# Kernel optimization log

Measured on AMD Instinct MI355X. Metric: run time of the kernel, lower is better.

Reference implementation:

```python
import jax, jax.numpy as jnp
import numpy as np

LN_EPS = 1e-6

def _layernorm(x, g, b):
    mu = jnp.mean(x, axis=-1, keepdims=True)
    var = jnp.mean((x - mu) ** 2, axis=-1, keepdims=True)
    return (x - mu) / jnp.sqrt(var + LN_EPS) * g + b

def _mha(q, k, v, wq, bq, wk, bk, wv, bv, fc, fcb, ln_g, ln_b, n_head, d_k, d_v):
    # standard post-LN multi-head attention (residual + layernorm), eval mode (no dropout)
    b, lq, _ = q.shape
    bk_, lk, _ = k.shape
    residual = q
    qh = (q @ wq + bq).reshape(b, lq, n_head, d_k).transpose(0, 2, 1, 3)      # [b,h,lq,dk]
    kh = (k @ wk + bk).reshape(bk_, lk, n_head, d_k).transpose(0, 2, 1, 3)    # [bk,h,lk,dk]
    vh = (v @ wv + bv).reshape(bk_, lk, n_head, d_v).transpose(0, 2, 1, 3)    # [bk,h,lk,dv]
    attn = jax.nn.softmax(jnp.matmul(qh, kh.swapaxes(-1, -2)) / (d_k ** 0.5), axis=-1)  # [b,h,lq,lk]
    out = jnp.matmul(attn, vh)                                                # [b,h,lq,dv]
    out = out.transpose(0, 2, 1, 3).reshape(b, lq, n_head * d_v)
    pre = out
    out = _layernorm(out @ fc + fcb + residual, ln_g, ln_b)
    return out, attn, pre


def setup_inputs() -> dict:
    key = jax.random.key(0)
    ks = jax.random.split(key, 32)
    B, C, H, W = 16, 64, 32, 32
    NC, D = 5, 96  # num_classes, memory feature dim
    s = 0.05
    d = {
        'x': jax.random.normal(ks[0], (B, C, H, W), jnp.float32),
        'memory': jax.random.normal(ks[1], (NC, D), jnp.float32),
        'wb_w': jax.random.normal(ks[2], (C, NC), jnp.float32) * s,
        'wb_b': jnp.zeros((NC,), jnp.float32),
        # slf_attn: n_head=1, d_model=64, d_input_k=96, d_k=96, d_v=64
        'a1_wq': jax.random.normal(ks[3], (64, 96), jnp.float32) * s,
        'a1_bq': jnp.zeros((96,), jnp.float32),
        'a1_wk': jax.random.normal(ks[4], (96, 96), jnp.float32) * s,
        'a1_bk': jnp.zeros((96,), jnp.float32),
        'a1_wv': jax.random.normal(ks[5], (96, 64), jnp.float32) * s,
        'a1_bv': jnp.zeros((64,), jnp.float32),
        'a1_fc': jax.random.normal(ks[6], (64, 64), jnp.float32) * s,
        'a1_fcb': jnp.zeros((64,), jnp.float32),
        'a1_ln_g': jnp.ones((64,), jnp.float32),
        'a1_ln_b': jnp.zeros((64,), jnp.float32),
        # slf_attn1: n_head=4, d_model=64, d_input_k=64, d_k=64, d_v=64
        'a2_wq': jax.random.normal(ks[7], (64, 256), jnp.float32) * s,
        'a2_bq': jnp.zeros((256,), jnp.float32),
        'a2_wk': jax.random.normal(ks[8], (64, 256), jnp.float32) * s,
        'a2_bk': jnp.zeros((256,), jnp.float32),
        'a2_wv': jax.random.normal(ks[9], (64, 256), jnp.float32) * s,
        'a2_bv': jnp.zeros((256,), jnp.float32),
        'a2_fc': jax.random.normal(ks[10], (256, 64), jnp.float32) * s,
        'a2_fcb': jnp.zeros((64,), jnp.float32),
        'a2_ln_g': jnp.ones((64,), jnp.float32),
        'a2_ln_b': jnp.zeros((64,), jnp.float32),
    }
    return d


def reference(x, memory, wb_w, wb_b,
              a1_wq, a1_bq, a1_wk, a1_bk, a1_wv, a1_bv, a1_fc, a1_fcb, a1_ln_g, a1_ln_b,
              a2_wq, a2_bq, a2_wk, a2_bk, a2_wv, a2_bv, a2_fc, a2_fcb, a2_ln_g, a2_ln_b):
    b, c, H, W = x.shape
    xt = x.transpose(0, 2, 3, 1).reshape(b, H * W, c)            # [b,HW,64]
    weight = xt @ wb_w + wb_b                                    # [b,HW,5]
    weight1 = jax.nn.softmax(weight, axis=-1)                    # softmax over classes
    weight2 = jax.nn.softmax(weight.transpose(0, 2, 1), axis=-1) # [b,5,HW], softmax over HW
    class_feat1 = jnp.matmul(weight2, xt)                        # [b,5,64] class-weighted pooling
    mem = memory[None]                                           # [1,5,96]
    cf, _, _ = _mha(class_feat1, mem, mem,
                    a1_wq, a1_bq, a1_wk, a1_bk, a1_wv, a1_bv, a1_fc, a1_fcb, a1_ln_g, a1_ln_b,
                    n_head=1, d_k=96, d_v=64)                    # [b,5,64]
    cf = jnp.matmul(weight1, cf)                                 # redistribution [b,HW,64]
    cf, _, _ = _mha(cf, cf, cf,
                    a2_wq, a2_bq, a2_wk, a2_bk, a2_wv, a2_bv, a2_fc, a2_fcb, a2_ln_g, a2_ln_b,
                    n_head=4, d_k=64, d_v=64)                    # [b,HW,64]
    return cf.transpose(0, 2, 1).reshape(-1, 64, H, W)           # [b,64,H,W]
```

## Files before the change

kernel.cpp:

```cpp
#include <hip/hip_runtime.h>
#include <math.h>

typedef unsigned short ushort_t;
typedef __attribute__((ext_vector_type(8))) short short8;
typedef __attribute__((ext_vector_type(4))) float f32x4;

#define B_  16
#define HW_ 1024
#define C_  64
#define NC_ 5
#define D1_ 96
#define NH_ 4
#define DH_ 64

#define MFMA32(A,B,C) __builtin_amdgcn_mfma_f32_16x16x32_bf16(A,B,C,0,0,0)

__device__ __forceinline__ ushort_t f2bf(float f) {
    unsigned u = __float_as_uint(f);
    u = u + 0x7fffu + ((u >> 16) & 1u);
    return (ushort_t)(u >> 16);
}

__device__ __forceinline__ unsigned pack2_trunc(float lo, float hi) {
    return (__float_as_uint(hi) & 0xffff0000u) | (__float_as_uint(lo) >> 16);
}
__device__ __forceinline__ float bf_lo(unsigned u) { return __uint_as_float(u << 16); }
__device__ __forceinline__ float bf_hi(unsigned u) { return __uint_as_float(u & 0xffff0000u); }

__global__ __launch_bounds__(64) void k1_logits(const float* __restrict__ x,
                                                const float* __restrict__ wb_w,
                                                const float* __restrict__ wb_b,
                                                float* __restrict__ logitsT,
                                                float* __restrict__ w1) {
    int b = blockIdx.x >> 4;
    int hw = (blockIdx.x & 15) * 64 + threadIdx.x;
    const float* xb = x + (size_t)b * C_ * HW_;
    float acc[NC_];
#pragma unroll
    for (int j = 0; j < NC_; j++) acc[j] = wb_b[j];
#pragma unroll 8
    for (int c = 0; c < C_; c++) {
        float xv = xb[c * HW_ + hw];
#pragma unroll
        for (int j = 0; j < NC_; j++) acc[j] += xv * wb_w[c * NC_ + j];
    }
    float m = acc[0];
#pragma unroll
    for (int j = 1; j < NC_; j++) m = fmaxf(m, acc[j]);
    float e[NC_], s = 0.f;
#pragma unroll
    for (int j = 0; j < NC_; j++) { e[j] = __expf(acc[j] - m); s += e[j]; }
    float inv = 1.f / s;
    int idx = b * HW_ + hw;
#pragma unroll
    for (int j = 0; j < NC_; j++) {
        logitsT[((size_t)b * NC_ + j) * HW_ + hw] = acc[j];
        w1[(size_t)idx * NC_ + j] = e[j] * inv;
    }
}

__global__ __launch_bounds__(256) void k2b_pool(const float* __restrict__ x,
                                                const float* __restrict__ logitsT,
                                                float* __restrict__ cf1) {
    __shared__ float pl[NC_ * HW_];
    __shared__ float sinv[NC_];
    int t = threadIdx.x;
    int b = blockIdx.x >> 4, chg = blockIdx.x & 15;
    const float* lp = logitsT + (size_t)b * NC_ * HW_;
    for (int i = t * 4; i < NC_ * HW_; i += 1024)
        *(float4*)(pl + i) = *(const float4*)(lp + i);
    __syncthreads();
    int w = t >> 6, lane = t & 63;
    for (int r = w; r < NC_; r += 4) {
        float m = -1e30f;
        for (int i = lane; i < HW_; i += 64) m = fmaxf(m, pl[r * HW_ + i]);
#pragma unroll
        for (int off = 1; off < 64; off <<= 1) m = fmaxf(m, __shfl_xor(m, off, 64));
        float s = 0.f;
        for (int i = lane; i < HW_; i += 64) {
            float e = __expf(pl[r * HW_ + i] - m);
            pl[r * HW_ + i] = e;
            s += e;
        }
#pragma unroll
        for (int off = 1; off < 64; off <<= 1) s += __shfl_xor(s, off, 64);
        if (lane == 0) sinv[r] = 1.f / s;
    }
    __syncthreads();
    int ch = chg * 4 + w;
    const float* xc = x + ((size_t)b * C_ + ch) * HW_;
    float acc[NC_] = {0.f, 0.f, 0.f, 0.f, 0.f};
#pragma unroll
    for (int i = 0; i < HW_ / 64; i++) {
        int hw = i * 64 + lane;
        float xv = xc[hw];
#pragma unroll
        for (int c = 0; c < NC_; c++) acc[c] += xv * pl[c * HW_ + hw];
    }
#pragma unroll
    for (int c = 0; c < NC_; c++) {
        float a = acc[c];
#pragma unroll
        for (int off = 1; off < 64; off <<= 1) a += __shfl_xor(a, off, 64);
        if (lane == 0) cf1[((size_t)b * NC_ + c) * C_ + ch] = a * sinv[c];
    }
}

__global__ __launch_bounds__(256) void k3_mha1(const float* __restrict__ cf1,
                                               const float* __restrict__ wq, const float* __restrict__ bq,
                                               const float* __restrict__ mem,
                                               const float* __restrict__ wk, const float* __restrict__ bk,
                                               const float* __restrict__ wv, const float* __restrict__ bv,
                                               const float* __restrict__ fc, const float* __restrict__ fcb,
                                               const float* __restrict__ lng, const float* __restrict__ lnb,
                                               float* __restrict__ cfs) {
    __shared__ float cs[NC_ * C_];
    __shared__ float kh[NC_ * D1_];
    __shared__ float vh[NC_ * DH_];
    __shared__ float q[NC_ * D1_];
    __shared__ float sc[NC_ * NC_];
    __shared__ float pp[NC_ * NC_];
    __shared__ float o[NC_ * C_];
    __shared__ float z[NC_ * C_];
    __shared__ float mu[NC_], rs[NC_];
    int t = threadIdx.x, b = blockIdx.x;
    for (int i = t; i < NC_ * C_; i += 256) cs[i] = cf1[(size_t)b * NC_ * C_ + i];
    for (int idx = t; idx < NC_ * D1_; idx += 256) {
        int i = idx / D1_, k = idx % D1_;
        float a = bk[k];
        for (int d = 0; d < D1_; d++) a += mem[i * D1_ + d] * wk[d * D1_ + k];
        kh[idx] = a;
    }
    for (int idx = t; idx < NC_ * DH_; idx += 256) {
        int i = idx / DH_, dv = idx % DH_;
        float a = bv[dv];
        for (int d = 0; d < D1_; d++) a += mem[i * D1_ + d] * wv[d * DH_ + dv];
        vh[idx] = a;
    }
    __syncthreads();
    for (int idx = t; idx < NC_ * D1_; idx += 256) {
        int i = idx / D1_, k = idx % D1_;
        float a = bq[k];
        for (int c = 0; c < C_; c++) a += cs[i * C_ + c] * wq[c * D1_ + k];
        q[idx] = a;
    }
    __syncthreads();
    if (t < NC_ * NC_) {
        int i = t / NC_, j = t % NC_;
        float a = 0.f;
        for (int k = 0; k < D1_; k++) a += q[i * D1_ + k] * kh[j * D1_ + k];
        sc[t] = a * 0.1020620726159657f;
    }
    __syncthreads();
    if (t < NC_) {
        float m = sc[t * NC_];
        for (int j = 1; j < NC_; j++) m = fmaxf(m, sc[t * NC_ + j]);
        float e[NC_], s = 0.f;
        for (int j = 0; j < NC_; j++) { e[j] = __expf(sc[t * NC_ + j] - m); s += e[j]; }
        float inv = 1.f / s;
        for (int j = 0; j < NC_; j++) pp[t * NC_ + j] = e[j] * inv;
    }
    __syncthreads();
    for (int idx = t; idx < NC_ * C_; idx += 256) {
        int i = idx / C_, dv = idx % C_;
        float a = 0.f;
        for (int j = 0; j < NC_; j++) a += pp[i * NC_ + j] * vh[j * C_ + dv];
        o[idx] = a;
    }
    __syncthreads();
    for (int idx = t; idx < NC_ * C_; idx += 256) {
        int i = idx / C_, dd = idx % C_;
        float a = fcb[dd] + cs[idx];
        for (int c2 = 0; c2 < C_; c2++) a += o[i * C_ + c2] * fc[c2 * C_ + dd];
        z[idx] = a;
    }
    __syncthreads();
    if (t < NC_) {
        float s = 0.f;
        for (int d = 0; d < C_; d++) s += z[t * C_ + d];
        float mm = s / C_;
        float v = 0.f;
        for (int d = 0; d < C_; d++) { float dd2 = z[t * C_ + d] - mm; v += dd2 * dd2; }
        mu[t] = mm; rs[t] = rsqrtf(v / C_ + 1e-6f);
    }
    __syncthreads();
    for (int idx = t; idx < NC_ * C_; idx += 256) {
        int i = idx / C_, dd = idx % C_;
        cfs[(size_t)b * NC_ * C_ + idx] = (z[idx] - mu[i]) * rs[i] * lng[dd] + lnb[dd];
    }
}

__global__ __launch_bounds__(256) void k5_proj(const float* __restrict__ w1,
                                               const float* __restrict__ cfs,
                                               const float* __restrict__ wq, const float* __restrict__ bq,
                                               const float* __restrict__ wk, const float* __restrict__ bk,
                                               const float* __restrict__ wv, const float* __restrict__ bv,
                                               ushort_t* __restrict__ Qb, ushort_t* __restrict__ Kb,
                                               ushort_t* __restrict__ Vt) {
    __shared__ float rows[8][64];
    int t = threadIdx.x;
    int which = blockIdx.y;
    int m0 = blockIdx.x * 8;
    int b5 = m0 >> 10;
    {
        int ch = t & 63, rr = t >> 6;
        const float* cp = cfs + (size_t)b5 * NC_ * C_;
        for (int r = rr; r < 8; r += 4) {
            const float* w1p = w1 + (size_t)(m0 + r) * NC_;
            float a = 0.f;
#pragma unroll
            for (int c = 0; c < NC_; c++) a += w1p[c] * cp[c * 64 + ch];
            rows[r][ch] = a;
        }
    }
    __syncthreads();
    const float* W = (which == 0) ? wq : (which == 1) ? wk : wv;
    const float* bias = (which == 0) ? bq : (which == 1) ? bk : bv;
    float scale = (which == 0) ? 0.18033688011112042f : 1.0f;
    int c = t;
    float bb = bias[c];
    float acc[8];
#pragma unroll
    for (int r = 0; r < 8; r++) acc[r] = bb;
    for (int k = 0; k < 64; k++) {
        float wv_ = W[k * 256 + c];
#pragma unroll
        for (int r = 0; r < 8; r++) acc[r] += rows[r][k] * wv_;
    }
    int h = c >> 6, dd = c & 63;
    if (which == 2) {
        union { ushort_t s[8]; uint4 u; } pk;
#pragma unroll
        for (int r = 0; r < 8; r++) pk.s[r] = f2bf(acc[r]);
        int l0 = m0 & 1023;
        *(uint4*)(Vt + ((size_t)(b5 * NH_ + h) * DH_ + dd) * HW_ + l0) = pk.u;
    } else {
        ushort_t* dst = (which == 0) ? Qb : Kb;
#pragma unroll
        for (int r = 0; r < 8; r++) {
            int m = m0 + r, b = m >> 10, hw = m & 1023;
            dst[(((size_t)(b * NH_ + h) * HW_) + hw) * DH_ + dd] = f2bf(acc[r] * scale);
        }
    }
}

__global__ __launch_bounds__(256) void k6_attn(const ushort_t* __restrict__ Qb,
                                               const ushort_t* __restrict__ Kb,
                                               const ushort_t* __restrict__ Vt,
                                               ushort_t* __restrict__ aoP0, ushort_t* __restrict__ aoP1,
                                               float* __restrict__ sP0, float* __restrict__ sP1) {
    int t = threadIdx.x;
    int w = t >> 6;
    int lane = t & 63;
    int l15 = lane & 15;
    int quad = lane >> 4;
    int L = blockIdx.x;
    int bh = ((L >> 3) & 7) * 8 + (L & 7);
    int khalf = (L >> 6) & 1;
    int qt = L >> 7;
    int b = bh >> 2, h = bh & 3;
    const ushort_t* Qp = Qb + (size_t)bh * HW_ * DH_;
    const ushort_t* Kp = Kb + (size_t)bh * HW_ * DH_;
    const ushort_t* Vp = Vt + (size_t)bh * DH_ * HW_;
    int row0 = qt * 256 + w * 16;
    short8 q0[4], q1[4];
#pragma unroll
    for (int tl = 0; tl < 4; tl++) {
        const ushort_t* qp = Qp + (size_t)(row0 + tl * 64 + l15) * DH_ + quad * 8;
        q0[tl] = *(const short8*)(qp);
        q1[tl] = *(const short8*)(qp + 32);
    }
    int f0 = ((l15 >> 2) * 8) + (l15 & 3);
    int kstart = khalf * 512;
    const ushort_t* K0p = Kp + (size_t)(kstart + f0) * DH_ + quad * 8;
    const ushort_t* K1p = Kp + (size_t)(kstart + f0 + 4) * DH_ + quad * 8;
    const ushort_t* Vp0 = Vp + (size_t)(0 * 16 + l15) * HW_ + kstart + quad * 8;
    const ushort_t* Vp1 = Vp + (size_t)(1 * 16 + l15) * HW_ + kstart + quad * 8;
    const ushort_t* Vp2 = Vp + (size_t)(2 * 16 + l15) * HW_ + kstart + quad * 8;
    const ushort_t* Vp3 = Vp + (size_t)(3 * 16 + l15) * HW_ + kstart + quad * 8;
    const short ONE = (short)0x3F80;
    short8 ones = {ONE, ONE, ONE, ONE, ONE, ONE, ONE, ONE};
    f32x4 o0[4], o1[4], o2[4], o3[4], oS[4];
#pragma unroll
    for (int tl = 0; tl < 4; tl++) {
        o0[tl] = (f32x4){0,0,0,0}; o1[tl] = (f32x4){0,0,0,0};
        o2[tl] = (f32x4){0,0,0,0}; o3[tl] = (f32x4){0,0,0,0};
        oS[tl] = (f32x4){0,0,0,0};
    }
    for (int kt = 0; kt < 16; kt++) {
        int kbase = kt * 32;
        size_t koff = (size_t)kbase * DH_;
        short8 ka0 = *(const short8*)(K0p + koff);
        short8 ka1 = *(const short8*)(K0p + koff + 32);
        short8 kb0 = *(const short8*)(K1p + koff);
        short8 kb1 = *(const short8*)(K1p + koff + 32);
        short8 v0 = *(const short8*)(Vp0 + kbase);
        short8 v1 = *(const short8*)(Vp1 + kbase);
        short8 v2 = *(const short8*)(Vp2 + kbase);
        short8 v3 = *(const short8*)(Vp3 + kbase);
        f32x4 z = {0,0,0,0};
#pragma unroll
        for (int tl = 0; tl < 4; tl++) {
            f32x4 s0 = MFMA32(ka0, q0[tl], z);  s0 = MFMA32(ka1, q1[tl], s0);
            f32x4 s1 = MFMA32(kb0, q0[tl], z);  s1 = MFMA32(kb1, q1[tl], s1);
            float p0 = exp2f(s0[0]), p1 = exp2f(s0[1]), p2 = exp2f(s0[2]), p3 = exp2f(s0[3]);
            float p4 = exp2f(s1[0]), p5 = exp2f(s1[1]), p6 = exp2f(s1[2]), p7 = exp2f(s1[3]);
            union { short8 v; unsigned u[4]; } pf;
            pf.u[0] = pack2_trunc(p0, p1);  pf.u[1] = pack2_trunc(p2, p3);
            pf.u[2] = pack2_trunc(p4, p5);  pf.u[3] = pack2_trunc(p6, p7);
            o0[tl] = MFMA32(v0, pf.v, o0[tl]);
            o1[tl] = MFMA32(v1, pf.v, o1[tl]);
            o2[tl] = MFMA32(v2, pf.v, o2[tl]);
            o3[tl] = MFMA32(v3, pf.v, o3[tl]);
            oS[tl] = MFMA32(ones, pf.v, oS[tl]);
        }
    }
    ushort_t* aoP = khalf ? aoP1 : aoP0;
    float* sP = khalf ? sP1 : sP0;
#pragma unroll
    for (int tl = 0; tl < 4; tl++) {
        int rowg = row0 + tl * 64 + l15;
        ushort_t* aop = aoP + ((size_t)(b * HW_ + rowg)) * 256 + h * 64 + quad * 4;
        uint2 u;
        u.x = pack2_trunc(o0[tl][0], o0[tl][1]); u.y = pack2_trunc(o0[tl][2], o0[tl][3]);
        *(uint2*)(aop + 0) = u;
        u.x = pack2_trunc(o1[tl][0], o1[tl][1]); u.y = pack2_trunc(o1[tl][2], o1[tl][3]);
        *(uint2*)(aop + 16) = u;
        u.x = pack2_trunc(o2[tl][0], o2[tl][1]); u.y = pack2_trunc(o2[tl][2], o2[tl][3]);
        *(uint2*)(aop + 32) = u;
        u.x = pack2_trunc(o3[tl][0], o3[tl][1]); u.y = pack2_trunc(o3[tl][2], o3[tl][3]);
        *(uint2*)(aop + 48) = u;
        if (quad == 0)
            sP[(size_t)(b * HW_ + rowg) * NH_ + h] = oS[tl][0];
    }
}

__global__ __launch_bounds__(256) void k7_final(const ushort_t* __restrict__ aoP0,
                                                const ushort_t* __restrict__ aoP1,
                                                const float* __restrict__ sP0,
                                                const float* __restrict__ sP1,
                                                const float* __restrict__ w1,
                                                const float* __restrict__ cfs,
                                                const float* __restrict__ fc, const float* __restrict__ fcb,
                                                const float* __restrict__ lng, const float* __restrict__ lnb,
                                                float* __restrict__ out) {
    __shared__ float srow[16 * 256];
    __shared__ float rinv[64];
    __shared__ float T[64 * 17];
    int t = threadIdx.x, w = t >> 6, d = t & 63;
    int m0 = blockIdx.x * 16;
    int b = m0 >> 10;
    if (t < 64) {
        int row = t >> 2, hh = t & 3;
        float s = sP0[(size_t)(m0 + row) * NH_ + hh] + sP1[(size_t)(m0 + row) * NH_ + hh];
        rinv[t] = 1.f / s;
    }
    __syncthreads();
    for (int i = t; i < 512; i += 256) {
        uint4 a  = *(const uint4*)(aoP0 + (size_t)m0 * 256 + i * 8);
        uint4 c4 = *(const uint4*)(aoP1 + (size_t)m0 * 256 + i * 8);
        int e = i * 8, row = e >> 8, hh = (e >> 6) & 3;
        float r = rinv[row * 4 + hh];
        srow[e + 0] = (bf_lo(a.x) + bf_lo(c4.x)) * r;
        srow[e + 1] = (bf_hi(a.x) + bf_hi(c4.x)) * r;
        srow[e + 2] = (bf_lo(a.y) + bf_lo(c4.y)) * r;
        srow[e + 3] = (bf_hi(a.y) + bf_hi(c4.y)) * r;
        srow[e + 4] = (bf_lo(a.z) + bf_lo(c4.z)) * r;
        srow[e + 5] = (bf_hi(a.z) + bf_hi(c4.z)) * r;
        srow[e + 6] = (bf_lo(a.w) + bf_lo(c4.w)) * r;
        srow[e + 7] = (bf_hi(a.w) + bf_hi(c4.w)) * r;
    }
    __syncthreads();
    float bias = fcb[d];
    const float* cp = cfs + (size_t)b * NC_ * C_;
    float a[4];
#pragma unroll
    for (int j = 0; j < 4; j++) {
        int m = m0 + w * 4 + j;
        const float* w1p = w1 + (size_t)m * NC_;
        float acc = bias;
#pragma unroll
        for (int c = 0; c < NC_; c++) acc += w1p[c] * cp[c * 64 + d];
        a[j] = acc;
    }
#pragma unroll 8
    for (int k = 0; k < 256; k++) {
        float f = fc[k * 64 + d];
#pragma unroll
        for (int j = 0; j < 4; j++) a[j] += srow[(w * 4 + j) * 256 + k] * f;
    }
    float g = lng[d], be = lnb[d];
#pragma unroll
    for (int j = 0; j < 4; j++) {
        float s1 = a[j], s2 = a[j] * a[j];
#pragma unroll
        for (int off = 1; off < 64; off <<= 1) {
            s1 += __shfl_xor(s1, off, 64);
            s2 += __shfl_xor(s2, off, 64);
        }
        float mu = s1 * (1.f / 64.f);
        float var = s2 * (1.f / 64.f) - mu * mu;
        float rstd = rsqrtf(var + 1e-6f);
        T[d * 17 + w * 4 + j] = (a[j] - mu) * rstd * g + be;
    }
    __syncthreads();
    int ch = t >> 2, part = t & 3;
    int hw0 = m0 & 1023;
    float4 v = {T[ch * 17 + part * 4 + 0], T[ch * 17 + part * 4 + 1],
                T[ch * 17 + part * 4 + 2], T[ch * 17 + part * 4 + 3]};
    *(float4*)&out[((size_t)b * 64 + ch) * 1024 + hw0 + part * 4] = v;
}

extern "C" void kernel_launch(void* const* d_in, const int* in_sizes, int n_in,
                              void* d_out, int out_size, void* d_ws, size_t ws_size,
                              hipStream_t stream) {
    const float* x      = (const float*)d_in[0];
    const float* memory = (const float*)d_in[1];
    const float* wb_w   = (const float*)d_in[2];
    const float* wb_b   = (const float*)d_in[3];
    const float* a1_wq  = (const float*)d_in[4];
    const float* a1_bq  = (const float*)d_in[5];
    const float* a1_wk  = (const float*)d_in[6];
    const float* a1_bk  = (const float*)d_in[7];
    const float* a1_wv  = (const float*)d_in[8];
    const float* a1_bv  = (const float*)d_in[9];
    const float* a1_fc  = (const float*)d_in[10];
    const float* a1_fcb = (const float*)d_in[11];
    const float* a1_ln_g = (const float*)d_in[12];
    const float* a1_ln_b = (const float*)d_in[13];
    const float* a2_wq  = (const float*)d_in[14];
    const float* a2_bq  = (const float*)d_in[15];
    const float* a2_wk  = (const float*)d_in[16];
    const float* a2_bk  = (const float*)d_in[17];
    const float* a2_wv  = (const float*)d_in[18];
    const float* a2_bv  = (const float*)d_in[19];
    const float* a2_fc  = (const float*)d_in[20];
    const float* a2_fcb = (const float*)d_in[21];
    const float* a2_ln_g = (const float*)d_in[22];
    const float* a2_ln_b = (const float*)d_in[23];

    float* ws = (float*)d_ws;
    float* logitsT = ws;
    float* w1  = logitsT + 81920;
    float* cf1 = w1 + 81920;
    float* cfs = cf1 + 5120;
    float* sP0 = cfs + 5120;
    float* sP1 = sP0 + 65536;
    ushort_t* aoP0 = (ushort_t*)(sP1 + 65536);
    ushort_t* aoP1 = aoP0 + 4194304;
    ushort_t* Qb = aoP1 + 4194304;
    ushort_t* Kb = Qb + 4194304;
    ushort_t* Vt = Kb + 4194304;

    k1_logits<<<256, 64, 0, stream>>>(x, wb_w, wb_b, logitsT, w1);
    k2b_pool<<<256, 256, 0, stream>>>(x, logitsT, cf1);
    k3_mha1<<<16, 256, 0, stream>>>(cf1, a1_wq, a1_bq, memory, a1_wk, a1_bk,
                                    a1_wv, a1_bv, a1_fc, a1_fcb,
                                    a1_ln_g, a1_ln_b, cfs);
    k5_proj<<<dim3(2048, 3), 256, 0, stream>>>(w1, cfs, a2_wq, a2_bq, a2_wk, a2_bk,
                                               a2_wv, a2_bv, Qb, Kb, Vt);
    k6_attn<<<512, 256, 0, stream>>>(Qb, Kb, Vt, aoP0, aoP1, sP0, sP1);
    k7_final<<<1024, 256, 0, stream>>>(aoP0, aoP1, sP0, sP1, w1, cfs, a2_fc, a2_fcb,
                                       a2_ln_g, a2_ln_b, (float*)d_out);
}
```

Before: 223.8 us.

## Rewrite QKV projection with bf16 MFMA tiles and vectorize fc reduction

Replaces the scalar FP32 QKV projection kernel, which handled 8 rows per block, with an MFMA-based kernel that handles 64 rows per block. Each block stages the redistributed activations and a bf16-transposed weight tile in shared memory, then issues 16x16x32 bf16 MFMAs, using a transposed operand arrangement for V so it can write Vt directly. Separately, the final kernel's fc reduction now reads srow as float4 and four fc values per step. The projection inputs are now rounded to bf16 before the matmul, which loses some precision, and each block reloads and converts the full weight matrix.

```diff
diff --git a/kernel.cpp b/kernel.cpp
--- a/kernel.cpp
+++ b/kernel.cpp
@@ -23,6 +23,9 @@
 
 __device__ __forceinline__ unsigned pack2_trunc(float lo, float hi) {
     return (__float_as_uint(hi) & 0xffff0000u) | (__float_as_uint(lo) >> 16);
+}
+__device__ __forceinline__ unsigned pack2_rne(float lo, float hi) {
+    return ((unsigned)f2bf(hi) << 16) | (unsigned)f2bf(lo);
 }
 __device__ __forceinline__ float bf_lo(unsigned u) { return __uint_as_float(u << 16); }
 __device__ __forceinline__ float bf_hi(unsigned u) { return __uint_as_float(u & 0xffff0000u); }
@@ -190,56 +193,101 @@
     }
 }
 
-__global__ __launch_bounds__(256) void k5_proj(const float* __restrict__ w1,
+__global__ __launch_bounds__(256) void k5_mfma(const float* __restrict__ w1,
                                                const float* __restrict__ cfs,
                                                const float* __restrict__ wq, const float* __restrict__ bq,
                                                const float* __restrict__ wk, const float* __restrict__ bk,
                                                const float* __restrict__ wv, const float* __restrict__ bv,
                                                ushort_t* __restrict__ Qb, ushort_t* __restrict__ Kb,
                                                ushort_t* __restrict__ Vt) {
-    __shared__ float rows[8][64];
+    __shared__ ushort_t Af[64][68];
+    __shared__ ushort_t Wt[256][68];
     int t = threadIdx.x;
     int which = blockIdx.y;
-    int m0 = blockIdx.x * 8;
-    int b5 = m0 >> 10;
+    int m0 = blockIdx.x * 64;
+    int b = m0 >> 10, lbase = m0 & 1023;
     {
-        int ch = t & 63, rr = t >> 6;
-        const float* cp = cfs + (size_t)b5 * NC_ * C_;
-        for (int r = rr; r < 8; r += 4) {
-            const float* w1p = w1 + (size_t)(m0 + r) * NC_;
-            float a = 0.f;
-#pragma unroll
-            for (int c = 0; c < NC_; c++) a += w1p[c] * cp[c * 64 + ch];
-            rows[r][ch] = a;
-        }
-    }
-    __syncthreads();
+        int r = t >> 2, ks = (t & 3) * 16;
+        const float* cp = cfs + (size_t)b * NC_ * C_;
+        const float* w1p = w1 + (size_t)(m0 + r) * NC_;
+        float v0 = w1p[0], v1 = w1p[1], v2 = w1p[2], v3 = w1p[3], v4 = w1p[4];
+#pragma unroll
+        for (int j = 0; j < 16; j += 2) {
+            int k = ks + j;
+            float e0 = v0 * cp[k]       + v1 * cp[64 + k]     + v2 * cp[128 + k]
+                     + v3 * cp[192 + k] + v4 * cp[256 + k];
+            float e1 = v0 * cp[k + 1]     + v1 * cp[64 + k + 1] + v2 * cp[128 + k + 1]
+                     + v3 * cp[192 + k + 1] + v4 * cp[256 + k + 1];
+            *(unsigned*)&Af[r][k] = pack2_rne(e0, e1);
+        }
+    }
     const float* W = (which == 0) ? wq : (which == 1) ? wk : wv;
-    const float* bias = (which == 0) ? bq : (which == 1) ? bk : bv;
-    float scale = (which == 0) ? 0.18033688011112042f : 1.0f;
-    int c = t;
-    float bb = bias[c];
-    float acc[8];
-#pragma unroll
-    for (int r = 0; r < 8; r++) acc[r] = bb;
-    for (int k = 0; k < 64; k++) {
-        float wv_ = W[k * 256 + c];
-#pragma unroll
-        for (int r = 0; r < 8; r++) acc[r] += rows[r][k] * wv_;
-    }
-    int h = c >> 6, dd = c & 63;
-    if (which == 2) {
-        union { ushort_t s[8]; uint4 u; } pk;
-#pragma unroll
-        for (int r = 0; r < 8; r++) pk.s[r] = f2bf(acc[r]);
-        int l0 = m0 & 1023;
-        *(uint4*)(Vt + ((size_t)(b5 * NH_ + h) * DH_ + dd) * HW_ + l0) = pk.u;
+    {
+        int n = t;
+#pragma unroll
+        for (int k = 0; k < 64; k += 2) {
+            *(unsigned*)&Wt[n][k] = pack2_rne(W[k * 256 + n], W[(k + 1) * 256 + n]);
+        }
+    }
+    __syncthreads();
+    int lane = t & 63, w = t >> 6;
+    int l15 = lane & 15, quad = lane >> 4;
+    if (which < 2) {
+        const float* bias = (which == 0) ? bq : bk;
+        float scale = (which == 0) ? 0.18033688011112042f : 1.0f;
+        ushort_t* dst = (which == 0) ? Qb : Kb;
+        short8 a0[4], a1[4];
+#pragma unroll
+        for (int mi = 0; mi < 4; mi++) {
+            a0[mi] = *(const short8*)&Af[mi * 16 + l15][quad * 8];
+            a1[mi] = *(const short8*)&Af[mi * 16 + l15][32 + quad * 8];
+        }
+#pragma unroll
+        for (int nt = 0; nt < 4; nt++) {
+            int ni = w * 4 + nt;
+            short8 b0 = *(const short8*)&Wt[ni * 16 + l15][quad * 8];
+            short8 b1 = *(const short8*)&Wt[ni * 16 + l15][32 + quad * 8];
+            int n = ni * 16 + l15;
+            float bb = bias[n];
+            int h = n >> 6, dd = n & 63;
+#pragma unroll
+            for (int mi = 0; mi < 4; mi++) {
+                f32x4 z = {0, 0, 0, 0};
+                f32x4 dv4 = MFMA32(a0[mi], b0, z);
+                dv4 = MFMA32(a1[mi], b1, dv4);
+                size_t base = ((size_t)(b * NH_ + h) * HW_ + (lbase + mi * 16 + quad * 4)) * DH_ + dd;
+#pragma unroll
+                for (int r = 0; r < 4; r++)
+                    dst[base + (size_t)r * DH_] = f2bf((dv4[r] + bb) * scale);
+            }
+        }
     } else {
-        ushort_t* dst = (which == 0) ? Qb : Kb;
-#pragma unroll
-        for (int r = 0; r < 8; r++) {
-            int m = m0 + r, b = m >> 10, hw = m & 1023;
-            dst[(((size_t)(b * NH_ + h) * HW_) + hw) * DH_ + dd] = f2bf(acc[r] * scale);
+        short8 a0[4], a1[4];
+#pragma unroll
+        for (int mt = 0; mt < 4; mt++) {
+            int mi = w * 4 + mt;
+            a0[mt] = *(const short8*)&Wt[mi * 16 + l15][quad * 8];
+            a1[mt] = *(const short8*)&Wt[mi * 16 + l15][32 + quad * 8];
+        }
+#pragma unroll
+        for (int nt = 0; nt < 4; nt++) {
+            short8 b0 = *(const short8*)&Af[nt * 16 + l15][quad * 8];
+            short8 b1 = *(const short8*)&Af[nt * 16 + l15][32 + quad * 8];
+#pragma unroll
+            for (int mt = 0; mt < 4; mt++) {
+                int mi = w * 4 + mt;
+                f32x4 z = {0, 0, 0, 0};
+                f32x4 dv4 = MFMA32(a0[mt], b0, z);
+                dv4 = MFMA32(a1[mt], b1, dv4);
+                int h = mi >> 2;
+#pragma unroll
+                for (int r = 0; r < 4; r++) {
+                    int nw = mi * 16 + quad * 4 + r;
+                    int dv = nw & 63;
+                    Vt[((size_t)(b * NH_ + h) * DH_ + dv) * HW_ + lbase + nt * 16 + l15] =
+                        f2bf(dv4[r] + bv[nw]);
+                }
+            }
         }
     }
 }
@@ -383,11 +431,18 @@
         for (int c = 0; c < NC_; c++) acc += w1p[c] * cp[c * 64 + d];
         a[j] = acc;
     }
-#pragma unroll 8
-    for (int k = 0; k < 256; k++) {
-        float f = fc[k * 64 + d];
-#pragma unroll
-        for (int j = 0; j < 4; j++) a[j] += srow[(w * 4 + j) * 256 + k] * f;
+#pragma unroll 4
+    for (int k4 = 0; k4 < 64; k4++) {
+        int k = k4 * 4;
+        float f0 = fc[(k + 0) * 64 + d];
+        float f1 = fc[(k + 1) * 64 + d];
+        float f2 = fc[(k + 2) * 64 + d];
+        float f3 = fc[(k + 3) * 64 + d];
+#pragma unroll
+        for (int j = 0; j < 4; j++) {
+            float4 s = *(const float4*)&srow[(w * 4 + j) * 256 + k];
+            a[j] += s.x * f0 + s.y * f1 + s.z * f2 + s.w * f3;
+        }
     }
     float g = lng[d], be = lnb[d];
 #pragma unroll
@@ -457,8 +512,8 @@
     k3_mha1<<<16, 256, 0, stream>>>(cf1, a1_wq, a1_bq, memory, a1_wk, a1_bk,
                                     a1_wv, a1_bv, a1_fc, a1_fcb,
                                     a1_ln_g, a1_ln_b, cfs);
-    k5_proj<<<dim3(2048, 3), 256, 0, stream>>>(w1, cfs, a2_wq, a2_bq, a2_wk, a2_bk,
-                                               a2_wv, a2_bv, Qb, Kb, Vt);
+    k5_mfma<<<dim3(256, 3), 256, 0, stream>>>(w1, cfs, a2_wq, a2_bq, a2_wk, a2_bk,
+                                              a2_wv, a2_bv, Qb, Kb, Vt);
     k6_attn<<<512, 256, 0, stream>>>(Qb, Kb, Vt, aoP0, aoP1, sP0, sP1);
     k7_final<<<1024, 256, 0, stream>>>(aoP0, aoP1, sP0, sP1, w1, cfs, a2_fc, a2_fcb,
                                        a2_ln_g, a2_ln_b, (float*)d_out);
```

Result: faster. 202.5 us (-9.5%).
